# Kernel tuning notes

Hardware: AMD Instinct MI355X
Metric: run time of the kernel (lower is better)

The kernel has to match this reference:

```python
import jax, jax.numpy as jnp
import numpy as np

B, L, H, D, T = 8, 4096, 8, 128, 128  # batch, max_len, kv_heads, head_size, max_new_tokens


def setup_inputs() -> dict:
    key = jax.random.key(0)
    ks = jax.random.split(key, 6)
    return {
        "keys": jax.random.normal(ks[0], (B, L, H, D), dtype=jnp.float32),
        "values": jax.random.normal(ks[1], (B, L, H, D), dtype=jnp.float32),
        "lengths": jax.random.randint(ks[2], (B,), 0, 2048, dtype=jnp.int32),
        "new_keys": jax.random.normal(ks[3], (B, T, H, D), dtype=jnp.float32),
        "new_values": jax.random.normal(ks[4], (B, T, H, D), dtype=jnp.float32),
        "new_lengths": jax.random.randint(ks[5], (B,), 0, T, dtype=jnp.int32),
    }


def reference(keys, values, lengths, new_keys, new_values, new_lengths):
    max_new_tokens = new_values.shape[1]
    max_len = keys.shape[1]
    operands = (keys, values, lengths, new_keys, new_values, new_lengths)

    def specialized_path(ops):
        k, v, l, nk, nv, nl = ops
        batch_size = k.shape[0]
        batch_idx = jnp.arange(batch_size)
        pos_idx = l
        update_vals_k = nk[:, 0]
        update_vals_v = nv[:, 0]
        should_update = (nl == 1)[:, None, None]
        original_vals_k = k[batch_idx, pos_idx]
        original_vals_v = v[batch_idx, pos_idx]
        vals_to_set_k = jnp.where(should_update, update_vals_k, original_vals_k)
        vals_to_set_v = jnp.where(should_update, update_vals_v, original_vals_v)
        updated_k = k.at[batch_idx, pos_idx].set(vals_to_set_k)
        updated_v = v.at[batch_idx, pos_idx].set(vals_to_set_v)
        return (updated_k, updated_v)

    def general_path(ops):
        k, v, l, nk, nv, nl = ops
        batch_size = k.shape[0]
        b_coords, p_coords = jnp.indices((batch_size, max_len))
        lengths_b = l[:, None]
        new_lengths_b = nl[:, None]
        update_mask = (p_coords >= lengths_b) & (p_coords < lengths_b + new_lengths_b)
        source_indices = p_coords - lengths_b
        clipped_source_indices = jnp.clip(source_indices, 0, max_new_tokens - 1)
        values_to_write_k = nk[b_coords, clipped_source_indices]
        values_to_write_v = nv[b_coords, clipped_source_indices]
        broadcast_mask = update_mask[:, :, None, None]
        updated_k = jnp.where(broadcast_mask, values_to_write_k, k)
        updated_v = jnp.where(broadcast_mask, values_to_write_v, v)
        return (updated_k, updated_v)

    is_special_case = jnp.all(new_lengths <= 1)
    updated_keys, updated_values = jax.lax.cond(is_special_case, specialized_path, general_path, operands)
    updated_lengths = lengths + new_lengths
    return (updated_keys, updated_values, updated_lengths)
```

## Files before the change

kernel.cpp:

```cpp
#include <hip/hip_runtime.h>

constexpr int B = 8;
constexpr int L = 4096;
constexpr int H = 8;
constexpr int D = 128;
constexpr int T = 128;

constexpr int ROW   = H * D;
constexpr int ROW4  = ROW / 4;
constexpr long long KV_ELEMS = (long long)B * L * ROW;
constexpr long long TOTAL4   = KV_ELEMS / 4;

__global__ __launch_bounds__(256) void kv_cache_update(
    const float4* __restrict__ keys,
    const float4* __restrict__ values,
    const int*    __restrict__ lengths,
    const float4* __restrict__ new_keys,
    const float4* __restrict__ new_values,
    const int*    __restrict__ new_lengths,
    float4* __restrict__ out_k,
    float4* __restrict__ out_v,
    float*  __restrict__ out_len)
{
    const long long stride = (long long)gridDim.x * blockDim.x;
    for (long long i = (long long)blockIdx.x * blockDim.x + threadIdx.x;
         i < TOTAL4; i += stride) {
        const int row = (int)(i >> 8);
        const int c   = (int)(i & 255);
        const int b   = row >> 12;
        const int p   = row & 4095;

        const int l  = lengths[b];
        const int nl = new_lengths[b];

        float4 vk, vv;
        if (p >= l && p < l + nl) {
            const long long nidx = ((long long)(b * T + (p - l)) << 8) + c;
            vk = new_keys[nidx];
            vv = new_values[nidx];
        } else {
            vk = keys[i];
            vv = values[i];
        }
        out_k[i] = vk;
        out_v[i] = vv;
    }

    if (blockIdx.x == 0 && threadIdx.x < B) {
        const int b = threadIdx.x;
        out_len[b] = (float)(lengths[b] + new_lengths[b]);
    }
}

extern "C" void kernel_launch(void* const* d_in, const int* in_sizes, int n_in,
                              void* d_out, int out_size, void* d_ws, size_t ws_size,
                              hipStream_t stream)
{
    const float4* keys       = (const float4*)d_in[0];
    const float4* values     = (const float4*)d_in[1];
    const int*    lengths    = (const int*)   d_in[2];
    const float4* new_keys   = (const float4*)d_in[3];
    const float4* new_values = (const float4*)d_in[4];
    const int*    new_lengths= (const int*)   d_in[5];

    float* out   = (float*)d_out;
    float4* out_k = (float4*)out;
    float4* out_v = (float4*)(out + KV_ELEMS);
    float*  out_len = out + 2 * KV_ELEMS;

    kv_cache_update<<<2048, 256, 0, stream>>>(
        keys, values, lengths, new_keys, new_values, new_lengths,
        out_k, out_v, out_len);
}
```

Baseline: 105.3 us.

## Split KV update into a bulk copy kernel and a scatter patch kernel

Replaces the single per-element masked-select kernel with two launches. The first is a plain unrolled float4 copy of keys and values, with separate blocks assigned to each tensor and four loads issued before four stores. The second overwrites only the rows in [len, len+new_len) with the new tokens and writes the updated lengths. This drops the per-element index math, length loads and branch, and adds more loads in flight per thread. The cost is a second kernel launch and rewriting the patched rows after they have already been copied.

After: 145.1 us. 37.8% more time.

```diff
diff --git a/kernel.cpp b/kernel.cpp
--- a/kernel.cpp
+++ b/kernel.cpp
@@ -9,46 +9,66 @@
 constexpr int ROW   = H * D;
 constexpr int ROW4  = ROW / 4;
 constexpr long long KV_ELEMS = (long long)B * L * ROW;
-constexpr long long TOTAL4   = KV_ELEMS / 4;
+constexpr int TOTAL4 = (int)(KV_ELEMS / 4);
 
-__global__ __launch_bounds__(256) void kv_cache_update(
+constexpr int COPY_BLOCKS_PER_TENSOR = 2048;
+
+__global__ __launch_bounds__(256) void kv_copy(
     const float4* __restrict__ keys,
     const float4* __restrict__ values,
-    const int*    __restrict__ lengths,
+    float4* __restrict__ out_k,
+    float4* __restrict__ out_v)
+{
+    const float4* __restrict__ src;
+    float4* __restrict__ dst;
+    int bid;
+    if (blockIdx.x < COPY_BLOCKS_PER_TENSOR) {
+        src = keys;   dst = out_k; bid = blockIdx.x;
+    } else {
+        src = values; dst = out_v; bid = blockIdx.x - COPY_BLOCKS_PER_TENSOR;
+    }
+
+    const int stride = COPY_BLOCKS_PER_TENSOR * 256;
+    int i = bid * 256 + (int)threadIdx.x;
+
+    #pragma unroll
+    for (int outer = 0; outer < 4; ++outer) {
+        float4 a = src[i];
+        float4 b = src[i + stride];
+        float4 c = src[i + 2 * stride];
+        float4 d = src[i + 3 * stride];
+        dst[i]              = a;
+        dst[i + stride]     = b;
+        dst[i + 2 * stride] = c;
+        dst[i + 3 * stride] = d;
+        i += 4 * stride;
+    }
+}
+
+__global__ __launch_bounds__(256) void kv_patch(
     const float4* __restrict__ new_keys,
     const float4* __restrict__ new_values,
+    const int*    __restrict__ lengths,
     const int*    __restrict__ new_lengths,
     float4* __restrict__ out_k,
     float4* __restrict__ out_v,
     float*  __restrict__ out_len)
 {
-    const long long stride = (long long)gridDim.x * blockDim.x;
-    for (long long i = (long long)blockIdx.x * blockDim.x + threadIdx.x;
-         i < TOTAL4; i += stride) {
-        const int row = (int)(i >> 8);
-        const int c   = (int)(i & 255);
-        const int b   = row >> 12;
-        const int p   = row & 4095;
+    const int b = blockIdx.x >> 7;
+    const int t = blockIdx.x & (T - 1);
 
-        const int l  = lengths[b];
-        const int nl = new_lengths[b];
-
-        float4 vk, vv;
-        if (p >= l && p < l + nl) {
-            const long long nidx = ((long long)(b * T + (p - l)) << 8) + c;
-            vk = new_keys[nidx];
-            vv = new_values[nidx];
-        } else {
-            vk = keys[i];
-            vv = values[i];
-        }
-        out_k[i] = vk;
-        out_v[i] = vv;
+    if (t < new_lengths[b]) {
+        const int l = lengths[b];
+        const int c = threadIdx.x;
+        const long long srci = ((long long)(b * T + t) << 8) + c;
+        const long long dsti = ((long long)(b * L + l + t) << 8) + c;
+        out_k[dsti] = new_keys[srci];
+        out_v[dsti] = new_values[srci];
     }
 
     if (blockIdx.x == 0 && threadIdx.x < B) {
-        const int b = threadIdx.x;
-        out_len[b] = (float)(lengths[b] + new_lengths[b]);
+        const int bb = threadIdx.x;
+        out_len[bb] = (float)(lengths[bb] + new_lengths[bb]);
     }
 }
 
@@ -63,12 +83,13 @@
     const float4* new_values = (const float4*)d_in[4];
     const int*    new_lengths= (const int*)   d_in[5];
 
-    float* out   = (float*)d_out;
-    float4* out_k = (float4*)out;
-    float4* out_v = (float4*)(out + KV_ELEMS);
+    float*  out     = (float*)d_out;
+    float4* out_k   = (float4*)out;
+    float4* out_v   = (float4*)(out + KV_ELEMS);
     float*  out_len = out + 2 * KV_ELEMS;
 
-    kv_cache_update<<<2048, 256, 0, stream>>>(
-        keys, values, lengths, new_keys, new_values, new_lengths,
-        out_k, out_v, out_len);
+    kv_copy<<<2 * COPY_BLOCKS_PER_TENSOR, 256, 0, stream>>>(keys, values, out_k, out_v);
+
+    kv_patch<<<B * T, 256, 0, stream>>>(new_keys, new_values, lengths, new_lengths,
+                                        out_k, out_v, out_len);
 }
```
